# Optimization experiments

Hardware: AMD Instinct MI355X
Metric: run time of the kernel (lower is better)

Reference implementation:

```python
import jax, jax.numpy as jnp
import numpy as np

B, CIN, COUT, N = 8, 64, 64, 4096
MODES, L, M = 64, 100, 20


def _cc_nodes_weights(m):
    # Clenshaw-Curtis nodes cos(k*pi/n) and weights on [-1, 1]
    n = m - 1
    k = np.arange(m)
    nodes = np.cos(np.pi * k / n)
    v = np.ones(m)
    for j in range(1, n // 2 + 1):
        b = 1.0 if 2 * j == n else 2.0
        v -= b / (4.0 * j * j - 1.0) * np.cos(2.0 * j * k * np.pi / n)
    w = 2.0 * v / n
    w[0] *= 0.5
    w[-1] *= 0.5
    return nodes, w


def setup_inputs() -> dict:
    key = jax.random.key(0)
    k1, k2, k3 = jax.random.split(key, 3)
    scale = 1.0 / (CIN * COUT)
    x = jax.random.normal(k1, (B, CIN, N), dtype=jnp.float32)
    w_real = scale * jax.random.uniform(k2, (CIN, COUT, MODES), dtype=jnp.float32)
    w_imag = scale * jax.random.uniform(k3, (CIN, COUT, MODES), dtype=jnp.float32)
    return {"x": x, "w_real": w_real, "w_imag": w_imag}


def _forward(x, w_real, w_imag):
    b, c, n = x.shape
    t = jnp.linspace(0.0, 1.0, n)
    f = np.fft.fftfreq(n, d=1.0 / n).astype(np.float32)  # integer freqs, fft order
    nodes, cw = _cc_nodes_weights(M)

    # ---- CFT: X(f) = sum_{segments l, cheb nodes k} w_lk * x(t_lk) * exp(-2i*pi*f*t_lk)
    h = 0.5 / L                               # segment half-width on [0,1]
    cents = (np.arange(L) + 0.5) / L
    t_nodes = (cents[:, None] + h * nodes[None, :]).ravel().astype(np.float32)  # (L*M,)
    wts = np.broadcast_to(h * cw, (L, M)).ravel().astype(np.float32)            # (L*M,)
    tq = jnp.asarray(t_nodes)
    # interpolate each (b, c) signal onto the Chebyshev quadrature nodes
    xs = jax.vmap(lambda s: jnp.interp(tq, t, s))(x.reshape(b * c, n))  # (BC, LM)
    phase = -2.0 * jnp.pi * jnp.asarray(f)[:, None] * tq[None, :]       # (N, LM)
    E = jnp.exp(1j * phase).astype(jnp.complex64) * jnp.asarray(wts)[None, :]
    x_cft = (xs.astype(jnp.complex64) @ E.T).reshape(b, c, n)           # (B, Cin, N)

    # ---- spectral channel mixing on lowest MODES fft-order frequencies
    w = (w_real + 1j * w_imag).astype(jnp.complex64)
    out_low = jnp.einsum('bix,iox->box', x_cft[:, :, :MODES], w)
    out_ft = jnp.concatenate(
        [out_low, jnp.zeros((b, COUT, n - MODES), dtype=jnp.complex64)], axis=-1)

    # ---- ICFT: x(t) = int X(f) exp(+2i*pi*f*t) df via the same segment quadrature
    order = np.argsort(f)
    f_sorted = f[order]
    cs = out_ft[:, :, jnp.asarray(order)].reshape(b * COUT, n)
    fa, fb = float(f_sorted[0]), float(f_sorted[-1])
    hf = (fb - fa) / (2.0 * L)
    fc = fa + (np.arange(L) + 0.5) * (fb - fa) / L
    f_nodes = (fc[:, None] + hf * nodes[None, :]).ravel().astype(np.float32)
    wfs = np.broadcast_to(hf * cw, (L, M)).ravel().astype(np.float32)
    fq = jnp.asarray(f_nodes)
    fs = jnp.asarray(f_sorted)
    ci = jax.vmap(lambda cv: jnp.interp(fq, fs, cv.real)
                  + 1j * jnp.interp(fq, fs, cv.imag))(cs)               # (BC, LM)
    phase2 = 2.0 * jnp.pi * fq[:, None] * t[None, :]                     # (LM, N)
    E2 = jnp.exp(1j * phase2).astype(jnp.complex64) * jnp.asarray(wfs)[:, None]
    return (ci.astype(jnp.complex64) @ E2).real.reshape(b, COUT, n)


def reference(x, w_real, w_imag):
    return _forward(x, w_real, w_imag)
```

## Files before the change

kernel.cpp:

```cpp
#include <hip/hip_runtime.h>


#define NN 4096
#define C1_19 0.9863613034027223
#define NS3 33
#define NSP 40

#define OFF_XRE 0
#define OFF_XIM 32768
#define OFF_Z   65536
#define OFF_P   106496

__device__ __forceinline__ float sin_rev(float r) { return __builtin_amdgcn_sinf(r); }
__device__ __forceinline__ float cos_rev(float r) { return __builtin_amdgcn_cosf(r); }

__device__ __forceinline__ void build_tables(double* nd, double* cwd, int t) {
    if (t == 0) {
        nd[0] = 1.0; nd[1] = C1_19;
        for (int k = 2; k < 20; ++k) nd[k] = 2.0 * C1_19 * nd[k - 1] - nd[k - 2];
    }
    __syncthreads();
    if (t < 20) {
        double v = 1.0;
        for (int j = 1; j <= 9; ++j) {
            int q = (2 * j * t) % 38; if (q > 19) q = 38 - q;
            v -= 2.0 / (4.0 * j * j - 1.0) * nd[q];
        }
        double w = 2.0 * v / 19.0;
        if (t == 0 || t == 19) w *= 0.5;
        cwd[t] = w;
    }
}

__global__ __launch_bounds__(256) void k_stage1(const float* __restrict__ x,
                                                float* __restrict__ P) {
    __shared__ double nd[20], cwd[20];
    __shared__ float qt[40], qa[40], qw[40];
    __shared__ int   qi[40];
    __shared__ __align__(16) float xw[32][93];
    __shared__ __align__(16) float e[2][40][64];
    __shared__ __align__(16) float xqT[40][32];
    const int t = threadIdx.x;
    const int sc = blockIdx.x, cc = blockIdx.y;
    build_tables(nd, cwd, t);
    __syncthreads();
    int i0 = (int)(81.9 * (double)sc) - 2;
    if (i0 < 0) i0 = 0;
    i0 &= ~3;
    if (i0 > 4004) i0 = 4004;
    if (t < 40) {
        int l = 2 * sc + (t >= 20), jn = t % 20;
        double tq = 0.005 * ((double)(2 * l + 1) + nd[jn]);
        double sf = tq * 4095.0;
        int i = (int)sf; if (i > 4094) i = 4094;
        double a = sf - (double)i;
        if (a < 0.0) a = 0.0; if (a > 1.0) a = 1.0;
        qi[t] = i - i0;
        qa[t] = (float)a;
        qt[t] = (float)tq;
        qw[t] = (float)(0.005 * cwd[jn]);
    }
    __syncthreads();
    for (int idx = t; idx < 32 * 23; idx += 256) {
        int row = idx / 23, c4 = idx % 23;
        float4 v = *(const float4*)&x[(size_t)(cc * 32 + row) * NN + i0 + c4 * 4];
        float* d = &xw[row][c4 * 4];
        d[0] = v.x; d[1] = v.y; d[2] = v.z; d[3] = v.w;
    }
    __syncthreads();
    for (int idx = t; idx < 40 * 64; idx += 256) {
        int s = idx >> 6, m = idx & 63;
        double r = -(double)m * (double)qt[s];
        r -= floor(r);
        float fr = (float)r;
        e[0][s][m] = qw[s] * cos_rev(fr);
        e[1][s][m] = qw[s] * sin_rev(fr);
    }
    for (int idx = t; idx < 40 * 32; idx += 256) {
        int q = idx >> 5, r = idx & 31;
        float a = qa[q];
        xqT[q][r] = (1.f - a) * xw[r][qi[q]] + a * xw[r][qi[q] + 1];
    }
    __syncthreads();
    const int mg = t & 15, bg = t >> 4;
    float aR[2][4] = {{0.f}}, aI[2][4] = {{0.f}};
    for (int s = 0; s < 40; ++s) {
        const float2 xv = *(const float2*)&xqT[s][bg * 2];
        const float4 er = *(const float4*)&e[0][s][mg * 4];
        const float4 ei = *(const float4*)&e[1][s][mg * 4];
#pragma unroll
        for (int p = 0; p < 2; ++p) {
            const float xm = p ? xv.y : xv.x;
            aR[p][0] += xm * er.x; aR[p][1] += xm * er.y;
            aR[p][2] += xm * er.z; aR[p][3] += xm * er.w;
            aI[p][0] += xm * ei.x; aI[p][1] += xm * ei.y;
            aI[p][2] += xm * ei.z; aI[p][3] += xm * ei.w;
        }
    }
#pragma unroll
    for (int p = 0; p < 2; ++p) {
        const size_t row = (size_t)sc * 512 + cc * 32 + bg * 2 + p;
        float4 vr, vi;
        vr.x = aR[p][0]; vr.y = aR[p][1]; vr.z = aR[p][2]; vr.w = aR[p][3];
        vi.x = aI[p][0]; vi.y = aI[p][1]; vi.z = aI[p][2]; vi.w = aI[p][3];
        *(float4*)&P[row * 128 + mg * 4]      = vr;
        *(float4*)&P[row * 128 + 64 + mg * 4] = vi;
    }
}

__global__ __launch_bounds__(256) void k_reduce(float* __restrict__ ws,
                                                const float* __restrict__ P) {
    __shared__ float4 red[8][32];
    const int t = threadIdx.x;
    const int grp = t >> 5, o = t & 31;
    const int oid = blockIdx.x * 32 + o;
    const float4* P4 = (const float4*)P;
    float4 s = {0.f, 0.f, 0.f, 0.f};
    for (int kk = grp; kk < 50; kk += 8) {
        float4 v = P4[(size_t)kk * 16384 + oid];
        s.x += v.x; s.y += v.y; s.z += v.z; s.w += v.w;
    }
    red[grp][o] = s;
    __syncthreads();
    if (t < 32) {
        float4 r = red[0][t];
#pragma unroll
        for (int g = 1; g < 8; ++g) {
            float4 v = red[g][t];
            r.x += v.x; r.y += v.y; r.z += v.z; r.w += v.w;
        }
        int od = blockIdx.x * 32 + t;
        int bc = od >> 5, c4 = od & 31;
        if (c4 < 16) *(float4*)&ws[OFF_XRE + (size_t)bc * 64 + c4 * 4] = r;
        else         *(float4*)&ws[OFF_XIM + (size_t)bc * 64 + (c4 - 16) * 4] = r;
    }
}

__global__ __launch_bounds__(256) void k_mixZ(const float* __restrict__ wr,
                                              const float* __restrict__ wi,
                                              float* __restrict__ ws) {
    __shared__ double nd[20], cwd[20];
    __shared__ float part[4][2][64];
    __shared__ float yt[2][64];
    __shared__ float sw0[NS3], sw1[NS3];
    __shared__ int   si0[NS3], si1[NS3];
    const int t = threadIdx.x;
    const int b = blockIdx.x >> 6, o = blockIdx.x & 63;
    build_tables(nd, cwd, t);
    __syncthreads();
    if (t < NS3) {
        int l = (t < 2) ? 49 : (t < 22 ? 50 : 51);
        int k = (t < 2) ? t : (t < 22 ? t - 2 : t - 13);
        double fq = -2048.0 + ((double)l + 0.5) * 40.95 + 20.475 * nd[k];
        int m0 = (int)floor(fq);
        float fr = (float)(fq - (double)m0);
        sw0[t] = (m0 >= 0 && m0 <= 63) ? (1.f - fr) : 0.f;
        sw1[t] = (m0 + 1 >= 0 && m0 + 1 <= 63) ? fr : 0.f;
        si0[t] = min(max(m0, 0), 63);
        si1[t] = min(max(m0 + 1, 0), 63);
    }
    const int m = t & 63, grp = t >> 6;
    float yr = 0.f, yi = 0.f;
#pragma unroll 4
    for (int i = grp * 16; i < grp * 16 + 16; ++i) {
        float xr = ws[OFF_XRE + (size_t)(b * 64 + i) * 64 + m];
        float xi = ws[OFF_XIM + (size_t)(b * 64 + i) * 64 + m];
        float a = wr[((size_t)i * 64 + o) * 64 + m];
        float c = wi[((size_t)i * 64 + o) * 64 + m];
        yr += xr * a - xi * c;
        yi += xr * c + xi * a;
    }
    part[grp][0][m] = yr;
    part[grp][1][m] = yi;
    __syncthreads();
    if (t < 128) {
        int pr = t >> 6, mm = t & 63;
        yt[pr][mm] = ((part[0][pr][mm] + part[1][pr][mm]) +
                      (part[2][pr][mm] + part[3][pr][mm]));
    }
    __syncthreads();
    if (t < 2 * NS3) {
        int p = t >= NS3, s = t - p * NS3;
        float z = sw0[s] * yt[p][si0[s]] + sw1[s] * yt[p][si1[s]];
        ws[OFF_Z + (size_t)p * 512 * NSP + ((size_t)b * 64 + o) * NSP + s] = z;
    } else if (t < 2 * NS3 + 14) {
        int u = t - 2 * NS3;
        int p = u / 7, s = NS3 + u % 7;
        ws[OFF_Z + (size_t)p * 512 * NSP + ((size_t)b * 64 + o) * NSP + s] = 0.f;
    }
}

__global__ __launch_bounds__(256) void k_stage3(const float* __restrict__ ws,
                                                float* __restrict__ out) {
    __shared__ double nd[20], cwd[20];
    __shared__ double sfq[NS3];
    __shared__ float  swf[NS3];
    __shared__ __align__(16) float zt[2][64][41];
    __shared__ __align__(16) float e2[2][NSP][64];
    const int t = threadIdx.x;
    const int jt = blockIdx.x, pc = blockIdx.y;
    build_tables(nd, cwd, t);
    __syncthreads();
    if (t < NS3) {
        int l = (t < 2) ? 49 : (t < 22 ? 50 : 51);
        int k = (t < 2) ? t : (t < 22 ? t - 2 : t - 13);
        sfq[t] = -2048.0 + ((double)l + 0.5) * 40.95 + 20.475 * nd[k];
        swf[t] = (float)(20.475 * cwd[k]);
    }
    for (int idx = t; idx < 2 * 64 * NSP; idx += 256) {
        int part = idx / (64 * NSP), rem = idx % (64 * NSP);
        int row = rem / NSP, s = rem % NSP;
        zt[part][row][s] =
            ws[OFF_Z + (size_t)part * 512 * NSP + ((size_t)pc * 64 + row) * NSP + s];
    }
    __syncthreads();
    const double inv4095 = 1.0 / 4095.0;
    for (int idx = t; idx < NSP * 64; idx += 256) {
        int s = idx >> 6, jl = idx & 63;
        float cr = 0.f, ci = 0.f;
        if (s < NS3) {
            double ph = sfq[s] * ((double)(jt * 64 + jl) * inv4095);
            ph -= floor(ph);
            float fr = (float)ph;
            cr = swf[s] * cos_rev(fr);
            ci = swf[s] * sin_rev(fr);
        }
        e2[0][s][jl] = cr;
        e2[1][s][jl] = ci;
    }
    __syncthreads();
    const int jg = t & 15, pg = t >> 4;
    float acc[4][4] = {{0.f}};
    for (int s0 = 0; s0 < NSP; s0 += 8) {
        float zr[4][8], zi[4][8];
#pragma unroll
        for (int p = 0; p < 4; ++p)
#pragma unroll
            for (int u = 0; u < 8; ++u) {
                zr[p][u] = zt[0][pg * 4 + p][s0 + u];
                zi[p][u] = zt[1][pg * 4 + p][s0 + u];
            }
#pragma unroll
        for (int u = 0; u < 8; ++u) {
            const float4 er = *(const float4*)&e2[0][s0 + u][jg * 4];
            const float4 ei = *(const float4*)&e2[1][s0 + u][jg * 4];
#pragma unroll
            for (int p = 0; p < 4; ++p) {
                acc[p][0] += zr[p][u] * er.x - zi[p][u] * ei.x;
                acc[p][1] += zr[p][u] * er.y - zi[p][u] * ei.y;
                acc[p][2] += zr[p][u] * er.z - zi[p][u] * ei.z;
                acc[p][3] += zr[p][u] * er.w - zi[p][u] * ei.w;
            }
        }
    }
#pragma unroll
    for (int p = 0; p < 4; ++p) {
        float4 r;
        r.x = acc[p][0]; r.y = acc[p][1]; r.z = acc[p][2]; r.w = acc[p][3];
        *(float4*)&out[(size_t)(pc * 64 + pg * 4 + p) * NN + jt * 64 + jg * 4] = r;
    }
}

extern "C" void kernel_launch(void* const* d_in, const int* in_sizes, int n_in,
                              void* d_out, int out_size, void* d_ws, size_t ws_size,
                              hipStream_t stream) {
    const float* x  = (const float*)d_in[0];
    const float* wr = (const float*)d_in[1];
    const float* wi = (const float*)d_in[2];
    float* out = (float*)d_out;
    float* ws  = (float*)d_ws;
    (void)in_sizes; (void)n_in; (void)out_size; (void)ws_size;

    float* P = ws + OFF_P;
    k_stage1<<<dim3(50, 16), 256, 0, stream>>>(x, P);
    k_reduce<<<512, 256, 0, stream>>>(ws, P);
    k_mixZ<<<512, 256, 0, stream>>>(wr, wi, ws);
    k_stage3<<<dim3(64, 8), 256, 0, stream>>>(ws, out);
}
```

Before: 37.14 us.

## Fuse CFT stage and reduction into one per-signal kernel using phase factorization

Replaces the two-kernel forward transform (segment-partial GEMM writing partials to workspace, then a separate reduction) with a single kernel where each block handles one (b,c) signal. The block loads the full signal into shared memory and factors the exponential as a per-segment twiddle times a shared 20-node table. Each thread contracts 20 nodes per segment and applies the segment twiddle, and a small shared-memory reduction combines the four segment groups. This removes one launch and the partial-sum round trip through global memory. In exchange each block reloads a whole 16KB row and does more trig work per segment.

```diff
diff --git a/kernel.cpp b/kernel.cpp
--- a/kernel.cpp
+++ b/kernel.cpp
@@ -9,7 +9,6 @@
 #define OFF_XRE 0
 #define OFF_XIM 32768
 #define OFF_Z   65536
-#define OFF_P   106496
 
 __device__ __forceinline__ float sin_rev(float r) { return __builtin_amdgcn_sinf(r); }
 __device__ __forceinline__ float cos_rev(float r) { return __builtin_amdgcn_cosf(r); }
@@ -32,107 +31,80 @@
     }
 }
 
-__global__ __launch_bounds__(256) void k_stage1(const float* __restrict__ x,
-                                                float* __restrict__ P) {
+__global__ __launch_bounds__(256) void k_cft(const float* __restrict__ x,
+                                             float* __restrict__ ws) {
     __shared__ double nd[20], cwd[20];
-    __shared__ float qt[40], qa[40], qw[40];
-    __shared__ int   qi[40];
-    __shared__ __align__(16) float xw[32][93];
-    __shared__ __align__(16) float e[2][40][64];
-    __shared__ __align__(16) float xqT[40][32];
+    __shared__ __align__(16) float xs[NN];
+    __shared__ __align__(16) float xq[2000];
+    __shared__ __align__(16) float Fri[20][64][2];
+    __shared__ float red[4][64][2];
     const int t = threadIdx.x;
-    const int sc = blockIdx.x, cc = blockIdx.y;
+    const int bc = blockIdx.x;
     build_tables(nd, cwd, t);
-    __syncthreads();
-    int i0 = (int)(81.9 * (double)sc) - 2;
-    if (i0 < 0) i0 = 0;
-    i0 &= ~3;
-    if (i0 > 4004) i0 = 4004;
-    if (t < 40) {
-        int l = 2 * sc + (t >= 20), jn = t % 20;
-        double tq = 0.005 * ((double)(2 * l + 1) + nd[jn]);
-        double sf = tq * 4095.0;
-        int i = (int)sf; if (i > 4094) i = 4094;
-        double a = sf - (double)i;
-        if (a < 0.0) a = 0.0; if (a > 1.0) a = 1.0;
-        qi[t] = i - i0;
-        qa[t] = (float)a;
-        qt[t] = (float)tq;
-        qw[t] = (float)(0.005 * cwd[jn]);
-    }
-    __syncthreads();
-    for (int idx = t; idx < 32 * 23; idx += 256) {
-        int row = idx / 23, c4 = idx % 23;
-        float4 v = *(const float4*)&x[(size_t)(cc * 32 + row) * NN + i0 + c4 * 4];
-        float* d = &xw[row][c4 * 4];
-        d[0] = v.x; d[1] = v.y; d[2] = v.z; d[3] = v.w;
-    }
-    __syncthreads();
-    for (int idx = t; idx < 40 * 64; idx += 256) {
-        int s = idx >> 6, m = idx & 63;
-        double r = -(double)m * (double)qt[s];
+#pragma unroll
+    for (int it = 0; it < 4; ++it) {
+        int c4 = it * 256 + t;
+        *(float4*)&xs[c4 * 4] = *(const float4*)&x[(size_t)bc * NN + c4 * 4];
+    }
+    __syncthreads();
+    for (int idx = t; idx < 1280; idx += 256) {
+        int k = idx >> 6, m = idx & 63;
+        double r = -0.005 * nd[k] * (double)m;
         r -= floor(r);
         float fr = (float)r;
-        e[0][s][m] = qw[s] * cos_rev(fr);
-        e[1][s][m] = qw[s] * sin_rev(fr);
-    }
-    for (int idx = t; idx < 40 * 32; idx += 256) {
-        int q = idx >> 5, r = idx & 31;
-        float a = qa[q];
-        xqT[q][r] = (1.f - a) * xw[r][qi[q]] + a * xw[r][qi[q] + 1];
-    }
-    __syncthreads();
-    const int mg = t & 15, bg = t >> 4;
-    float aR[2][4] = {{0.f}}, aI[2][4] = {{0.f}};
-    for (int s = 0; s < 40; ++s) {
-        const float2 xv = *(const float2*)&xqT[s][bg * 2];
-        const float4 er = *(const float4*)&e[0][s][mg * 4];
-        const float4 ei = *(const float4*)&e[1][s][mg * 4];
-#pragma unroll
-        for (int p = 0; p < 2; ++p) {
-            const float xm = p ? xv.y : xv.x;
-            aR[p][0] += xm * er.x; aR[p][1] += xm * er.y;
-            aR[p][2] += xm * er.z; aR[p][3] += xm * er.w;
-            aI[p][0] += xm * ei.x; aI[p][1] += xm * ei.y;
-            aI[p][2] += xm * ei.z; aI[p][3] += xm * ei.w;
-        }
-    }
-#pragma unroll
-    for (int p = 0; p < 2; ++p) {
-        const size_t row = (size_t)sc * 512 + cc * 32 + bg * 2 + p;
-        float4 vr, vi;
-        vr.x = aR[p][0]; vr.y = aR[p][1]; vr.z = aR[p][2]; vr.w = aR[p][3];
-        vi.x = aI[p][0]; vi.y = aI[p][1]; vi.z = aI[p][2]; vi.w = aI[p][3];
-        *(float4*)&P[row * 128 + mg * 4]      = vr;
-        *(float4*)&P[row * 128 + 64 + mg * 4] = vi;
-    }
-}
-
-__global__ __launch_bounds__(256) void k_reduce(float* __restrict__ ws,
-                                                const float* __restrict__ P) {
-    __shared__ float4 red[8][32];
-    const int t = threadIdx.x;
-    const int grp = t >> 5, o = t & 31;
-    const int oid = blockIdx.x * 32 + o;
-    const float4* P4 = (const float4*)P;
-    float4 s = {0.f, 0.f, 0.f, 0.f};
-    for (int kk = grp; kk < 50; kk += 8) {
-        float4 v = P4[(size_t)kk * 16384 + oid];
-        s.x += v.x; s.y += v.y; s.z += v.z; s.w += v.w;
-    }
-    red[grp][o] = s;
-    __syncthreads();
-    if (t < 32) {
-        float4 r = red[0][t];
-#pragma unroll
-        for (int g = 1; g < 8; ++g) {
-            float4 v = red[g][t];
-            r.x += v.x; r.y += v.y; r.z += v.z; r.w += v.w;
-        }
-        int od = blockIdx.x * 32 + t;
-        int bc = od >> 5, c4 = od & 31;
-        if (c4 < 16) *(float4*)&ws[OFF_XRE + (size_t)bc * 64 + c4 * 4] = r;
-        else         *(float4*)&ws[OFF_XIM + (size_t)bc * 64 + (c4 - 16) * 4] = r;
+        float w = (float)(0.005 * cwd[k]);
+        Fri[k][m][0] = w * cos_rev(fr);
+        Fri[k][m][1] = w * sin_rev(fr);
+    }
+#pragma unroll
+    for (int it = 0; it < 8; ++it) {
+        int node = it * 256 + t;
+        if (node < 2000) {
+            int l = node / 20, k = node - l * 20;
+            double tq = 0.005 * ((double)(2 * l + 1) + nd[k]);
+            double sf = tq * 4095.0;
+            int i = (int)sf; if (i > 4094) i = 4094;
+            double a = sf - (double)i;
+            if (a < 0.0) a = 0.0; if (a > 1.0) a = 1.0;
+            float af = (float)a;
+            xq[node] = (1.f - af) * xs[i] + af * xs[i + 1];
+        }
+    }
+    __syncthreads();
+    const int m = t & 63, grp = t >> 6;
+    float Fre[20], Fim[20];
+#pragma unroll
+    for (int k = 0; k < 20; ++k) {
+        Fre[k] = Fri[k][m][0];
+        Fim[k] = Fri[k][m][1];
+    }
+    float ar = 0.f, ai = 0.f;
+    for (int l = grp * 25; l < grp * 25 + 25; ++l) {
+        const float4* q4 = (const float4*)&xq[l * 20];
+        float ur = 0.f, ui = 0.f;
+#pragma unroll
+        for (int c = 0; c < 5; ++c) {
+            float4 q = q4[c];
+            ur += q.x * Fre[c * 4]     + q.y * Fre[c * 4 + 1]
+                + q.z * Fre[c * 4 + 2] + q.w * Fre[c * 4 + 3];
+            ui += q.x * Fim[c * 4]     + q.y * Fim[c * 4 + 1]
+                + q.z * Fim[c * 4 + 2] + q.w * Fim[c * 4 + 3];
+        }
+        double r = -(double)(m * (2 * l + 1)) / 200.0;
+        r -= floor(r);
+        float fr = (float)r;
+        float tr = cos_rev(fr), ti = sin_rev(fr);
+        ar += tr * ur - ti * ui;
+        ai += tr * ui + ti * ur;
+    }
+    red[grp][m][0] = ar;
+    red[grp][m][1] = ai;
+    __syncthreads();
+    if (t < 64) {
+        float sr = (red[0][t][0] + red[1][t][0]) + (red[2][t][0] + red[3][t][0]);
+        float si = (red[0][t][1] + red[1][t][1]) + (red[2][t][1] + red[3][t][1]);
+        ws[OFF_XRE + (size_t)bc * 64 + t] = sr;
+        ws[OFF_XIM + (size_t)bc * 64 + t] = si;
     }
 }
 
@@ -271,9 +243,7 @@
     float* ws  = (float*)d_ws;
     (void)in_sizes; (void)n_in; (void)out_size; (void)ws_size;
 
-    float* P = ws + OFF_P;
-    k_stage1<<<dim3(50, 16), 256, 0, stream>>>(x, P);
-    k_reduce<<<512, 256, 0, stream>>>(ws, P);
+    k_cft<<<512, 256, 0, stream>>>(x, ws);
     k_mixZ<<<512, 256, 0, stream>>>(wr, wi, ws);
     k_stage3<<<dim3(64, 8), 256, 0, stream>>>(ws, out);
 }
```

Measured after the change: 31.10 us. 16.3% less time.
